# Performance work log

Hardware: AMD Instinct MI355X
Metric: run time of the kernel (lower is better)

The kernel has to match this reference:

```python
import jax, jax.numpy as jnp
import numpy as np

N_EMBD = 1024
N_HEAD = 16


def setup_inputs() -> dict:
    key = jax.random.key(0)
    ks = jax.random.split(key, 9)
    s = 1.0 / np.sqrt(N_EMBD)
    d = {
        "x": jax.random.normal(ks[0], (4, 2048, N_EMBD), dtype=jnp.float32),
        "Wq": jax.random.normal(ks[1], (N_EMBD, N_EMBD), dtype=jnp.float32) * s,
        "bq": jnp.zeros((N_EMBD,), dtype=jnp.float32),
        "Wk": jax.random.normal(ks[2], (N_EMBD, N_EMBD), dtype=jnp.float32) * s,
        "bk": jnp.zeros((N_EMBD,), dtype=jnp.float32),
        "Wv": jax.random.normal(ks[3], (N_EMBD, N_EMBD), dtype=jnp.float32) * s,
        "bv": jnp.zeros((N_EMBD,), dtype=jnp.float32),
        "Wp": jax.random.normal(ks[4], (N_EMBD, N_EMBD), dtype=jnp.float32) * s,
        "bp": jnp.zeros((N_EMBD,), dtype=jnp.float32),
    }
    return d


def reference(x, Wq, bq, Wk, bk, Wv, bv, Wp, bp):
    B, T, C = x.shape
    H = N_HEAD
    D = C // H  # head dim
    # QKV projections -> [B, H, T, D]
    def split_heads(y):
        return y.reshape(B, T, H, D).transpose(0, 2, 1, 3)
    q = split_heads(x @ Wq + bq)
    k = split_heads(x @ Wk + bk)
    v = split_heads(x @ Wv + bv)
    # full (non-causal) attention, scaled by 1/sqrt(D)
    att = jnp.einsum("bhtd,bhsd->bhts", q, k) * (1.0 / np.sqrt(D))
    att = jax.nn.softmax(att, axis=-1)  # dropout is identity (p=0 / eval)
    out = jnp.einsum("bhts,bhsd->bhtd", att, v)
    out = out.transpose(0, 2, 1, 3).reshape(B, T, C)
    return out @ Wp + bp
```

## Files before the change

### kernel.cpp

```cpp
#include <hip/hip_runtime.h>
#include <math.h>

#define B_ 4
#define T_ 2048
#define C_ 1024
#define H_ 16
#define D_ 64
#define M_ (B_ * T_)

#define QSCALE 0.18033688011112042f

using bf16x8 = __attribute__((ext_vector_type(8))) short;
using f32x4  = __attribute__((ext_vector_type(4))) float;

__device__ __forceinline__ unsigned short f2bf(float f) {
  unsigned u = __float_as_uint(f);
  unsigned r = u + 0x7FFFu + ((u >> 16) & 1u);
  return (unsigned short)(r >> 16);
}
__device__ __forceinline__ float bf2f(unsigned short h) {
  return __uint_as_float(((unsigned)h) << 16);
}

__global__ __launch_bounds__(256) void conv_x(const float* __restrict__ x,
                                              unsigned short* __restrict__ hi,
                                              unsigned short* __restrict__ lo) {
  const size_t i = ((size_t)blockIdx.x * 256 + threadIdx.x) * 4;
  const float4 v = *(const float4*)&x[i];
  ushort4 h, l;
  h.x = f2bf(v.x); l.x = f2bf(v.x - bf2f(h.x));
  h.y = f2bf(v.y); l.y = f2bf(v.y - bf2f(h.y));
  h.z = f2bf(v.z); l.z = f2bf(v.z - bf2f(h.z));
  h.w = f2bf(v.w); l.w = f2bf(v.w - bf2f(h.w));
  *(ushort4*)&hi[i] = h;
  *(ushort4*)&lo[i] = l;
}

__global__ __launch_bounds__(256) void conv_wT(const float* __restrict__ W,
                                               unsigned short* __restrict__ hi,
                                               unsigned short* __restrict__ lo,
                                               int n_off) {
  __shared__ float t[64][65];
  const int k0 = blockIdx.y * 64, n0 = blockIdx.x * 64;
  const int lr = threadIdx.x >> 4;
  const int lc4 = (threadIdx.x & 15) * 4;
#pragma unroll
  for (int i = 0; i < 4; ++i) {
    const int r = lr + 16 * i;
    const float4 v = *(const float4*)&W[(size_t)(k0 + r) * 1024 + n0 + lc4];
    t[r][lc4 + 0] = v.x; t[r][lc4 + 1] = v.y;
    t[r][lc4 + 2] = v.z; t[r][lc4 + 3] = v.w;
  }
  __syncthreads();
#pragma unroll
  for (int i = 0; i < 4; ++i) {
    const int nr = lr + 16 * i;
    ushort4 h, l;
    float a0 = t[lc4 + 0][nr], a1 = t[lc4 + 1][nr];
    float a2 = t[lc4 + 2][nr], a3 = t[lc4 + 3][nr];
    h.x = f2bf(a0); l.x = f2bf(a0 - bf2f(h.x));
    h.y = f2bf(a1); l.y = f2bf(a1 - bf2f(h.y));
    h.z = f2bf(a2); l.z = f2bf(a2 - bf2f(h.z));
    h.w = f2bf(a3); l.w = f2bf(a3 - bf2f(h.w));
    const size_t o = (size_t)(n_off + n0 + nr) * 1024 + k0 + lc4;
    *(ushort4*)&hi[o] = h;
    *(ushort4*)&lo[o] = l;
  }
}

template <int MODE>
__global__ __launch_bounds__(256) void gemm_mfma(
    const unsigned short* __restrict__ Ahi, const unsigned short* __restrict__ Alo,
    const unsigned short* __restrict__ Bhi, const unsigned short* __restrict__ Blo,
    const float* __restrict__ bias0, const float* __restrict__ bias1,
    const float* __restrict__ bias2,
    void* P0, void* P1, void* P2, void* P3, void* P4, void* P5) {
  __shared__ __align__(16) unsigned short Als[128 * 32];
  __shared__ __align__(16) unsigned short Bls[128 * 32];

  const int tid = threadIdx.x;
  const int lane = tid & 63;
  const int wid = tid >> 6;
  const int m0 = blockIdx.y * 128, n0 = blockIdx.x * 128;
  const int wm = (wid >> 1) * 64, wn = (wid & 1) * 64;

  f32x4 acc[4][4] = {};

  const int srow = lane >> 2;
  const int sc = lane & 3;

  for (int k0 = 0; k0 < 3 * 1024; k0 += 32) {
    const int seg = k0 >> 10;
    const int kk = k0 & 1023;
    const unsigned short* ga = (seg == 2) ? Alo : Ahi;
    const unsigned short* gb = (seg == 1) ? Blo : Bhi;

    __syncthreads();
#pragma unroll
    for (int c = 0; c < 2; ++c) {
      const int chunk = wid * 2 + c;
      const int row = chunk * 16 + srow;
      const int kch = sc ^ ((row >> 1) & 3);
      {
        const unsigned short* src = ga + (size_t)(m0 + row) * 1024 + kk + kch * 8;
        __builtin_amdgcn_global_load_lds(
            (const __attribute__((address_space(1))) void*)src,
            (__attribute__((address_space(3))) void*)(Als + chunk * 512), 16, 0, 0);
      }
      {
        const unsigned short* src = gb + (size_t)(n0 + row) * 1024 + kk + kch * 8;
        __builtin_amdgcn_global_load_lds(
            (const __attribute__((address_space(1))) void*)src,
            (__attribute__((address_space(3))) void*)(Bls + chunk * 512), 16, 0, 0);
      }
    }
    __syncthreads();

    const int fr = lane & 15;
    const int q = lane >> 4;
    bf16x8 af[4], bfr[4];
#pragma unroll
    for (int i = 0; i < 4; ++i) {
      const int arow = wm + i * 16 + fr;
      af[i] = *(const bf16x8*)(Als + arow * 32 + (q ^ ((arow >> 1) & 3)) * 8);
      const int brow = wn + i * 16 + fr;
      bfr[i] = *(const bf16x8*)(Bls + brow * 32 + (q ^ ((brow >> 1) & 3)) * 8);
    }
#pragma unroll
    for (int i = 0; i < 4; ++i)
#pragma unroll
      for (int j = 0; j < 4; ++j)
        acc[i][j] = __builtin_amdgcn_mfma_f32_16x16x32_bf16(af[i], bfr[j], acc[i][j], 0, 0, 0);
  }

  const int fr = lane & 15;
  const int q = lane >> 4;
  if (MODE == 0) {
    float* out = (float*)P0;
#pragma unroll
    for (int i = 0; i < 4; ++i)
#pragma unroll
      for (int j = 0; j < 4; ++j)
#pragma unroll
        for (int r = 0; r < 4; ++r) {
          const int m = m0 + wm + i * 16 + q * 4 + r;
          const int n = n0 + wn + j * 16 + fr;
          out[(size_t)m * 1024 + n] = acc[i][j][r] + bias0[n];
        }
  } else {
#pragma unroll
    for (int i = 0; i < 4; ++i) {
#pragma unroll
      for (int j = 0; j < 4; ++j) {
        const int n = n0 + wn + j * 16 + fr;
        const int seg = n >> 10, ww = n & 1023, h = ww >> 6, d = ww & 63;
        const float bv = ((seg == 0) ? bias0 : (seg == 1) ? bias1 : bias2)[ww];
        const int mb = m0 + wm + i * 16 + q * 4;
        const int b = mb >> 11, t0 = mb & 2047;
        unsigned short hv[4], lv[4];
#pragma unroll
        for (int r = 0; r < 4; ++r) {
          float v = acc[i][j][r] + bv;
          if (seg == 0) v *= QSCALE;
          hv[r] = f2bf(v);
          lv[r] = f2bf(v - bf2f(hv[r]));
        }
        if (seg == 2) {
          const size_t o = (((size_t)b * H_ + h) * D_ + d) * T_ + t0;
          ushort4 h4, l4;
          h4.x = hv[0]; h4.y = hv[1]; h4.z = hv[2]; h4.w = hv[3];
          l4.x = lv[0]; l4.y = lv[1]; l4.z = lv[2]; l4.w = lv[3];
          *(ushort4*)&((unsigned short*)P4)[o] = h4;
          *(ushort4*)&((unsigned short*)P5)[o] = l4;
        } else {
          unsigned short* Hq = (unsigned short*)((seg == 0) ? P0 : P2);
          unsigned short* Lq = (unsigned short*)((seg == 0) ? P1 : P3);
          const size_t ob = ((size_t)b * H_ + h) * T_;
#pragma unroll
          for (int r = 0; r < 4; ++r) {
            const size_t o = (ob + t0 + r) * D_ + d;
            Hq[o] = hv[r];
            Lq[o] = lv[r];
          }
        }
      }
    }
  }
}

__global__ __launch_bounds__(256) void flash_mfma(
    const unsigned short* __restrict__ Qhi, const unsigned short* __restrict__ Qlo,
    const unsigned short* __restrict__ Khi, const unsigned short* __restrict__ Klo,
    const unsigned short* __restrict__ Vthi, const unsigned short* __restrict__ Vtlo,
    unsigned short* __restrict__ chi, unsigned short* __restrict__ clo) {
  __shared__ __align__(16) unsigned short KhiS[64 * 64];
  __shared__ __align__(16) unsigned short KloS[64 * 64];
  __shared__ __align__(16) unsigned short VhiS[64 * 64];
  __shared__ __align__(16) unsigned short VloS[64 * 64];
  __shared__ __align__(16) unsigned short Ps[4][32][80];

  const int tid = threadIdx.x;
  const int lane = tid & 63;
  const int w = tid >> 6;
  const int bh = blockIdx.y;
  const int b = bh >> 4, h = bh & 15;
  const int q0 = blockIdx.x * 128;
  const int fr = lane & 15, q = lane >> 4;

  const size_t kbase = (size_t)bh * T_ * D_;
  const size_t vbase = (size_t)bh * D_ * T_;

  bf16x8 qhi[2][2], qlo[2][2];
#pragma unroll
  for (int g = 0; g < 2; ++g)
#pragma unroll
    for (int ks = 0; ks < 2; ++ks) {
      const size_t a = kbase + (size_t)(q0 + w * 32 + g * 16 + fr) * D_ + ks * 32 + q * 8;
      qhi[g][ks] = *(const bf16x8*)(Qhi + a);
      qlo[g][ks] = *(const bf16x8*)(Qlo + a);
    }

  f32x4 accO[2][4] = {};
  float lsum[2][4] = {};

  for (int s0 = 0; s0 < T_; s0 += 64) {
    __syncthreads();
#pragma unroll
    for (int c = 0; c < 2; ++c) {
      const int ci = w * 128 + c * 64 + lane;
      const int row = ci >> 3, slot = ci & 7;
      const int kch = slot ^ (row & 7);
      const int ldsb = (w * 128 + c * 64) * 8;
      const unsigned short* sk = Khi + kbase + (size_t)(s0 + row) * D_ + kch * 8;
      __builtin_amdgcn_global_load_lds(
          (const __attribute__((address_space(1))) void*)sk,
          (__attribute__((address_space(3))) void*)(KhiS + ldsb), 16, 0, 0);
      const unsigned short* sk2 = Klo + kbase + (size_t)(s0 + row) * D_ + kch * 8;
      __builtin_amdgcn_global_load_lds(
          (const __attribute__((address_space(1))) void*)sk2,
          (__attribute__((address_space(3))) void*)(KloS + ldsb), 16, 0, 0);
      const unsigned short* sv = Vthi + vbase + (size_t)row * T_ + s0 + kch * 8;
      __builtin_amdgcn_global_load_lds(
          (const __attribute__((address_space(1))) void*)sv,
          (__attribute__((address_space(3))) void*)(VhiS + ldsb), 16, 0, 0);
      const unsigned short* sv2 = Vtlo + vbase + (size_t)row * T_ + s0 + kch * 8;
      __builtin_amdgcn_global_load_lds(
          (const __attribute__((address_space(1))) void*)sv2,
          (__attribute__((address_space(3))) void*)(VloS + ldsb), 16, 0, 0);
    }
    __syncthreads();

    f32x4 accS[2][4] = {};
#pragma unroll
    for (int j = 0; j < 4; ++j) {
      bf16x8 khf[2], klf[2];
#pragma unroll
      for (int ks = 0; ks < 2; ++ks) {
        const int rs = j * 16 + fr;
        const int off = rs * 64 + ((ks * 4 + q) ^ (rs & 7)) * 8;
        khf[ks] = *(const bf16x8*)(KhiS + off);
        klf[ks] = *(const bf16x8*)(KloS + off);
      }
#pragma unroll
      for (int g = 0; g < 2; ++g)
#pragma unroll
        for (int ks = 0; ks < 2; ++ks) {
          accS[g][j] = __builtin_amdgcn_mfma_f32_16x16x32_bf16(qhi[g][ks], khf[ks], accS[g][j], 0, 0, 0);
          accS[g][j] = __builtin_amdgcn_mfma_f32_16x16x32_bf16(qhi[g][ks], klf[ks], accS[g][j], 0, 0, 0);
          accS[g][j] = __builtin_amdgcn_mfma_f32_16x16x32_bf16(qlo[g][ks], khf[ks], accS[g][j], 0, 0, 0);
        }
    }

#pragma unroll
    for (int g = 0; g < 2; ++g)
#pragma unroll
      for (int j = 0; j < 4; ++j)
#pragma unroll
        for (int r = 0; r < 4; ++r) {
          const float p = __builtin_amdgcn_exp2f(accS[g][j][r]);
          lsum[g][r] += p;
          Ps[w][g * 16 + q * 4 + r][j * 16 + fr] = f2bf(p);
        }

    asm volatile("s_waitcnt lgkmcnt(0)" ::: "memory");
    __builtin_amdgcn_sched_barrier(0);

    bf16x8 pa[2][2];
#pragma unroll
    for (int g = 0; g < 2; ++g)
#pragma unroll
      for (int ks = 0; ks < 2; ++ks)
        pa[g][ks] = *(const bf16x8*)&Ps[w][g * 16 + fr][ks * 32 + q * 8];
#pragma unroll
    for (int j = 0; j < 4; ++j) {
      bf16x8 vh[2], vl[2];
#pragma unroll
      for (int ks = 0; ks < 2; ++ks) {
        const int rd = j * 16 + fr;
        const int off = rd * 64 + ((ks * 4 + q) ^ (rd & 7)) * 8;
        vh[ks] = *(const bf16x8*)(VhiS + off);
        vl[ks] = *(const bf16x8*)(VloS + off);
      }
#pragma unroll
      for (int g = 0; g < 2; ++g)
#pragma unroll
        for (int ks = 0; ks < 2; ++ks) {
          accO[g][j] = __builtin_amdgcn_mfma_f32_16x16x32_bf16(pa[g][ks], vh[ks], accO[g][j], 0, 0, 0);
          accO[g][j] = __builtin_amdgcn_mfma_f32_16x16x32_bf16(pa[g][ks], vl[ks], accO[g][j], 0, 0, 0);
        }
    }
  }

#pragma unroll
  for (int g = 0; g < 2; ++g) {
#pragma unroll
    for (int r = 0; r < 4; ++r) {
      float rs = lsum[g][r];
#pragma unroll
      for (int off = 1; off < 16; off <<= 1) rs += __shfl_xor(rs, off);
      const float inv = 1.0f / rs;
      const int t = q0 + w * 32 + g * 16 + q * 4 + r;
#pragma unroll
      for (int j = 0; j < 4; ++j) {
        const float v = accO[g][j][r] * inv;
        const unsigned short hv = f2bf(v);
        const unsigned short lv = f2bf(v - bf2f(hv));
        const size_t idx = ((size_t)b * T_ + t) * C_ + h * D_ + j * 16 + fr;
        chi[idx] = hv;
        clo[idx] = lv;
      }
    }
  }
}

extern "C" void kernel_launch(void* const* d_in, const int* in_sizes, int n_in,
                              void* d_out, int out_size, void* d_ws,
                              size_t ws_size, hipStream_t stream) {
  const float* x = (const float*)d_in[0];
  const float* Wq = (const float*)d_in[1];
  const float* bq = (const float*)d_in[2];
  const float* Wk = (const float*)d_in[3];
  const float* bk = (const float*)d_in[4];
  const float* Wv = (const float*)d_in[5];
  const float* bv = (const float*)d_in[6];
  const float* Wp = (const float*)d_in[7];
  const float* bp = (const float*)d_in[8];
  float* out = (float*)d_out;

  char* w = (char*)d_ws;
  unsigned short* xhi = (unsigned short*)w;     w += (size_t)M_ * C_ * 2;
  unsigned short* xlo = (unsigned short*)w;     w += (size_t)M_ * C_ * 2;
  unsigned short* Wqkv_hi = (unsigned short*)w; w += (size_t)3 * C_ * C_ * 2;
  unsigned short* Wqkv_lo = (unsigned short*)w; w += (size_t)3 * C_ * C_ * 2;
  unsigned short* Wp_hi = (unsigned short*)w;   w += (size_t)C_ * C_ * 2;
  unsigned short* Wp_lo = (unsigned short*)w;   w += (size_t)C_ * C_ * 2;
  unsigned short* Qhi = (unsigned short*)w;     w += (size_t)M_ * C_ * 2;
  unsigned short* Qlo = (unsigned short*)w;     w += (size_t)M_ * C_ * 2;
  unsigned short* Khi = (unsigned short*)w;     w += (size_t)M_ * C_ * 2;
  unsigned short* Klo = (unsigned short*)w;     w += (size_t)M_ * C_ * 2;
  unsigned short* Vthi = (unsigned short*)w;    w += (size_t)M_ * C_ * 2;
  unsigned short* Vtlo = (unsigned short*)w;    w += (size_t)M_ * C_ * 2;
  unsigned short* chi = (unsigned short*)w;     w += (size_t)M_ * C_ * 2;
  unsigned short* clo = (unsigned short*)w;     w += (size_t)M_ * C_ * 2;

  const dim3 blk(256);

  conv_x<<<dim3((M_ * C_) / (4 * 256)), blk, 0, stream>>>(x, xhi, xlo);
  conv_wT<<<dim3(16, 16), blk, 0, stream>>>(Wq, Wqkv_hi, Wqkv_lo, 0);
  conv_wT<<<dim3(16, 16), blk, 0, stream>>>(Wk, Wqkv_hi, Wqkv_lo, 1024);
  conv_wT<<<dim3(16, 16), blk, 0, stream>>>(Wv, Wqkv_hi, Wqkv_lo, 2048);
  conv_wT<<<dim3(16, 16), blk, 0, stream>>>(Wp, Wp_hi, Wp_lo, 0);

  gemm_mfma<1><<<dim3(3072 / 128, M_ / 128), blk, 0, stream>>>(
      xhi, xlo, Wqkv_hi, Wqkv_lo, bq, bk, bv,
      Qhi, Qlo, Khi, Klo, Vthi, Vtlo);

  flash_mfma<<<dim3(T_ / 128, B_ * H_), blk, 0, stream>>>(
      Qhi, Qlo, Khi, Klo, Vthi, Vtlo, chi, clo);

  gemm_mfma<0><<<dim3(1024 / 128, M_ / 128), blk, 0, stream>>>(
      chi, clo, Wp_hi, Wp_lo, bp, bp, bp,
      out, nullptr, nullptr, nullptr, nullptr, nullptr);

  (void)in_sizes; (void)n_in; (void)out_size; (void)ws_size;
}
```

Before: 552.9 us.

## Merge split-bf16 GEMM passes, swizzle block order, transpose attention MFMA operands

The GEMM now loads hi and lo tiles of A and B together and runs all three bf16 products in one K loop. A and B tiles are staged once instead of three times, at the cost of doubling LDS use and raising register pressure. Both the GEMM and the flash kernel remap block indices so neighbouring workgroups share data in cache. The flash kernel swaps MFMA operands to compute transposed S and O tiles, which allows packed bf16 conversion of P, swizzled P stores to LDS, a cheaper row-sum reduction and vectorised output stores.

```diff
diff --git a/kernel.cpp b/kernel.cpp
--- a/kernel.cpp
+++ b/kernel.cpp
@@ -20,6 +20,11 @@
 }
 __device__ __forceinline__ float bf2f(unsigned short h) {
   return __uint_as_float(((unsigned)h) << 16);
+}
+__device__ __forceinline__ unsigned cvtpk_bf16(float lo, float hi) {
+  unsigned r;
+  asm volatile("v_cvt_pk_bf16_f32 %0, %1, %2" : "=v"(r) : "v"(lo), "v"(hi));
+  return r;
 }
 
 __global__ __launch_bounds__(256) void conv_x(const float* __restrict__ x,
@@ -75,66 +80,91 @@
     const float* __restrict__ bias0, const float* __restrict__ bias1,
     const float* __restrict__ bias2,
     void* P0, void* P1, void* P2, void* P3, void* P4, void* P5) {
-  __shared__ __align__(16) unsigned short Als[128 * 32];
-  __shared__ __align__(16) unsigned short Bls[128 * 32];
+  __shared__ __align__(16) unsigned short AhS[128 * 32];
+  __shared__ __align__(16) unsigned short AlS[128 * 32];
+  __shared__ __align__(16) unsigned short BhS[128 * 32];
+  __shared__ __align__(16) unsigned short BlS[128 * 32];
 
   const int tid = threadIdx.x;
   const int lane = tid & 63;
   const int wid = tid >> 6;
-  const int m0 = blockIdx.y * 128, n0 = blockIdx.x * 128;
+
+  const int GX = (MODE == 1) ? 24 : 8;
+  const int nwg = GX * 64;
+  int lin = blockIdx.x + blockIdx.y * GX;
+  lin = (lin & 7) * (nwg >> 3) + (lin >> 3);
+  const int m0 = (lin / GX) * 128, n0 = (lin % GX) * 128;
+
   const int wm = (wid >> 1) * 64, wn = (wid & 1) * 64;
 
   f32x4 acc[4][4] = {};
 
   const int srow = lane >> 2;
   const int sc = lane & 3;
-
-  for (int k0 = 0; k0 < 3 * 1024; k0 += 32) {
-    const int seg = k0 >> 10;
-    const int kk = k0 & 1023;
-    const unsigned short* ga = (seg == 2) ? Alo : Ahi;
-    const unsigned short* gb = (seg == 1) ? Blo : Bhi;
-
+  const int fr = lane & 15;
+  const int q = lane >> 4;
+
+  for (int k0 = 0; k0 < 1024; k0 += 32) {
     __syncthreads();
 #pragma unroll
     for (int c = 0; c < 2; ++c) {
       const int chunk = wid * 2 + c;
       const int row = chunk * 16 + srow;
       const int kch = sc ^ ((row >> 1) & 3);
-      {
-        const unsigned short* src = ga + (size_t)(m0 + row) * 1024 + kk + kch * 8;
-        __builtin_amdgcn_global_load_lds(
-            (const __attribute__((address_space(1))) void*)src,
-            (__attribute__((address_space(3))) void*)(Als + chunk * 512), 16, 0, 0);
-      }
-      {
-        const unsigned short* src = gb + (size_t)(n0 + row) * 1024 + kk + kch * 8;
-        __builtin_amdgcn_global_load_lds(
-            (const __attribute__((address_space(1))) void*)src,
-            (__attribute__((address_space(3))) void*)(Bls + chunk * 512), 16, 0, 0);
-      }
+      const size_t ao = (size_t)(m0 + row) * 1024 + k0 + kch * 8;
+      const size_t bo = (size_t)(n0 + row) * 1024 + k0 + kch * 8;
+      __builtin_amdgcn_global_load_lds(
+          (const __attribute__((address_space(1))) void*)(Ahi + ao),
+          (__attribute__((address_space(3))) void*)(AhS + chunk * 512), 16, 0, 0);
+      __builtin_amdgcn_global_load_lds(
+          (const __attribute__((address_space(1))) void*)(Alo + ao),
+          (__attribute__((address_space(3))) void*)(AlS + chunk * 512), 16, 0, 0);
+      __builtin_amdgcn_global_load_lds(
+          (const __attribute__((address_space(1))) void*)(Bhi + bo),
+          (__attribute__((address_space(3))) void*)(BhS + chunk * 512), 16, 0, 0);
+      __builtin_amdgcn_global_load_lds(
+          (const __attribute__((address_space(1))) void*)(Blo + bo),
+          (__attribute__((address_space(3))) void*)(BlS + chunk * 512), 16, 0, 0);
     }
     __syncthreads();
 
-    const int fr = lane & 15;
-    const int q = lane >> 4;
-    bf16x8 af[4], bfr[4];
+    bf16x8 afh[4], bfh[4], afl[4], bfl[4];
 #pragma unroll
     for (int i = 0; i < 4; ++i) {
       const int arow = wm + i * 16 + fr;
-      af[i] = *(const bf16x8*)(Als + arow * 32 + (q ^ ((arow >> 1) & 3)) * 8);
+      const int aoff = arow * 32 + (q ^ ((arow >> 1) & 3)) * 8;
+      afh[i] = *(const bf16x8*)(AhS + aoff);
       const int brow = wn + i * 16 + fr;
-      bfr[i] = *(const bf16x8*)(Bls + brow * 32 + (q ^ ((brow >> 1) & 3)) * 8);
+      const int boff = brow * 32 + (q ^ ((brow >> 1) & 3)) * 8;
+      bfh[i] = *(const bf16x8*)(BhS + boff);
     }
 #pragma unroll
     for (int i = 0; i < 4; ++i)
 #pragma unroll
       for (int j = 0; j < 4; ++j)
-        acc[i][j] = __builtin_amdgcn_mfma_f32_16x16x32_bf16(af[i], bfr[j], acc[i][j], 0, 0, 0);
-  }
-
-  const int fr = lane & 15;
-  const int q = lane >> 4;
+        acc[i][j] = __builtin_amdgcn_mfma_f32_16x16x32_bf16(afh[i], bfh[j], acc[i][j], 0, 0, 0);
+#pragma unroll
+    for (int i = 0; i < 4; ++i) {
+      const int brow = wn + i * 16 + fr;
+      bfl[i] = *(const bf16x8*)(BlS + brow * 32 + (q ^ ((brow >> 1) & 3)) * 8);
+    }
+#pragma unroll
+    for (int i = 0; i < 4; ++i)
+#pragma unroll
+      for (int j = 0; j < 4; ++j)
+        acc[i][j] = __builtin_amdgcn_mfma_f32_16x16x32_bf16(afh[i], bfl[j], acc[i][j], 0, 0, 0);
+#pragma unroll
+    for (int i = 0; i < 4; ++i) {
+      const int arow = wm + i * 16 + fr;
+      afl[i] = *(const bf16x8*)(AlS + arow * 32 + (q ^ ((arow >> 1) & 3)) * 8);
+    }
+#pragma unroll
+    for (int i = 0; i < 4; ++i)
+#pragma unroll
+      for (int j = 0; j < 4; ++j)
+        acc[i][j] = __builtin_amdgcn_mfma_f32_16x16x32_bf16(afl[i], bfh[j], acc[i][j], 0, 0, 0);
+  }
+
   if (MODE == 0) {
     float* out = (float*)P0;
 #pragma unroll
@@ -197,14 +227,18 @@
   __shared__ __align__(16) unsigned short KloS[64 * 64];
   __shared__ __align__(16) unsigned short VhiS[64 * 64];
   __shared__ __align__(16) unsigned short VloS[64 * 64];
-  __shared__ __align__(16) unsigned short Ps[4][32][80];
+  __shared__ __align__(16) unsigned short PsT[4][32 * 64];
 
   const int tid = threadIdx.x;
   const int lane = tid & 63;
   const int w = tid >> 6;
-  const int bh = blockIdx.y;
+
+  int lin = blockIdx.x + blockIdx.y * 16;
+  lin = (lin & 7) * 128 + (lin >> 3);
+  const int bh = lin >> 4;
+  const int q0 = (lin & 15) * 128;
+
   const int b = bh >> 4, h = bh & 15;
-  const int q0 = blockIdx.x * 128;
   const int fr = lane & 15, q = lane >> 4;
 
   const size_t kbase = (size_t)bh * T_ * D_;
@@ -220,8 +254,10 @@
       qlo[g][ks] = *(const bf16x8*)(Qlo + a);
     }
 
-  f32x4 accO[2][4] = {};
-  float lsum[2][4] = {};
+  unsigned short* psw = &PsT[w][0];
+
+  f32x4 accO[4][2] = {};
+  float lsum[2] = {};
 
   for (int s0 = 0; s0 < T_; s0 += 64) {
     __syncthreads();
@@ -250,13 +286,13 @@
     }
     __syncthreads();
 
-    f32x4 accS[2][4] = {};
-#pragma unroll
-    for (int j = 0; j < 4; ++j) {
+    f32x4 accS[4][2] = {};
+#pragma unroll
+    for (int sj = 0; sj < 4; ++sj) {
       bf16x8 khf[2], klf[2];
 #pragma unroll
       for (int ks = 0; ks < 2; ++ks) {
-        const int rs = j * 16 + fr;
+        const int rs = sj * 16 + fr;
         const int off = rs * 64 + ((ks * 4 + q) ^ (rs & 7)) * 8;
         khf[ks] = *(const bf16x8*)(KhiS + off);
         klf[ks] = *(const bf16x8*)(KloS + off);
@@ -265,32 +301,41 @@
       for (int g = 0; g < 2; ++g)
 #pragma unroll
         for (int ks = 0; ks < 2; ++ks) {
-          accS[g][j] = __builtin_amdgcn_mfma_f32_16x16x32_bf16(qhi[g][ks], khf[ks], accS[g][j], 0, 0, 0);
-          accS[g][j] = __builtin_amdgcn_mfma_f32_16x16x32_bf16(qhi[g][ks], klf[ks], accS[g][j], 0, 0, 0);
-          accS[g][j] = __builtin_amdgcn_mfma_f32_16x16x32_bf16(qlo[g][ks], khf[ks], accS[g][j], 0, 0, 0);
+          accS[sj][g] = __builtin_amdgcn_mfma_f32_16x16x32_bf16(khf[ks], qhi[g][ks], accS[sj][g], 0, 0, 0);
+          accS[sj][g] = __builtin_amdgcn_mfma_f32_16x16x32_bf16(khf[ks], qlo[g][ks], accS[sj][g], 0, 0, 0);
+          accS[sj][g] = __builtin_amdgcn_mfma_f32_16x16x32_bf16(klf[ks], qhi[g][ks], accS[sj][g], 0, 0, 0);
         }
     }
 
 #pragma unroll
-    for (int g = 0; g < 2; ++g)
-#pragma unroll
-      for (int j = 0; j < 4; ++j)
-#pragma unroll
-        for (int r = 0; r < 4; ++r) {
-          const float p = __builtin_amdgcn_exp2f(accS[g][j][r]);
-          lsum[g][r] += p;
-          Ps[w][g * 16 + q * 4 + r][j * 16 + fr] = f2bf(p);
-        }
+    for (int g = 0; g < 2; ++g) {
+      const int qc = g * 16 + fr;
+#pragma unroll
+      for (int sj = 0; sj < 4; ++sj) {
+        const float p0 = __builtin_amdgcn_exp2f(accS[sj][g][0]);
+        const float p1 = __builtin_amdgcn_exp2f(accS[sj][g][1]);
+        const float p2 = __builtin_amdgcn_exp2f(accS[sj][g][2]);
+        const float p3 = __builtin_amdgcn_exp2f(accS[sj][g][3]);
+        lsum[g] += (p0 + p1) + (p2 + p3);
+        uint2 pk;
+        pk.x = cvtpk_bf16(p0, p1);
+        pk.y = cvtpk_bf16(p2, p3);
+        const int off = (qc * 128 + sj * 32 + q * 8) ^ ((fr & 7) << 4);
+        *(uint2*)((char*)psw + off) = pk;
+      }
+    }
 
     asm volatile("s_waitcnt lgkmcnt(0)" ::: "memory");
     __builtin_amdgcn_sched_barrier(0);
 
-    bf16x8 pa[2][2];
+    bf16x8 pb[2][2];
 #pragma unroll
     for (int g = 0; g < 2; ++g)
 #pragma unroll
-      for (int ks = 0; ks < 2; ++ks)
-        pa[g][ks] = *(const bf16x8*)&Ps[w][g * 16 + fr][ks * 32 + q * 8];
+      for (int ks = 0; ks < 2; ++ks) {
+        const int off = ((g * 16 + fr) * 128 + ks * 64 + q * 16) ^ ((fr & 7) << 4);
+        pb[g][ks] = *(const bf16x8*)((char*)psw + off);
+      }
 #pragma unroll
     for (int j = 0; j < 4; ++j) {
       bf16x8 vh[2], vl[2];
@@ -305,30 +350,32 @@
       for (int g = 0; g < 2; ++g)
 #pragma unroll
         for (int ks = 0; ks < 2; ++ks) {
-          accO[g][j] = __builtin_amdgcn_mfma_f32_16x16x32_bf16(pa[g][ks], vh[ks], accO[g][j], 0, 0, 0);
-          accO[g][j] = __builtin_amdgcn_mfma_f32_16x16x32_bf16(pa[g][ks], vl[ks], accO[g][j], 0, 0, 0);
+          accO[j][g] = __builtin_amdgcn_mfma_f32_16x16x32_bf16(vh[ks], pb[g][ks], accO[j][g], 0, 0, 0);
+          accO[j][g] = __builtin_amdgcn_mfma_f32_16x16x32_bf16(vl[ks], pb[g][ks], accO[j][g], 0, 0, 0);
         }
     }
   }
 
 #pragma unroll
   for (int g = 0; g < 2; ++g) {
-#pragma unroll
-    for (int r = 0; r < 4; ++r) {
-      float rs = lsum[g][r];
-#pragma unroll
-      for (int off = 1; off < 16; off <<= 1) rs += __shfl_xor(rs, off);
-      const float inv = 1.0f / rs;
-      const int t = q0 + w * 32 + g * 16 + q * 4 + r;
-#pragma unroll
-      for (int j = 0; j < 4; ++j) {
-        const float v = accO[g][j][r] * inv;
-        const unsigned short hv = f2bf(v);
-        const unsigned short lv = f2bf(v - bf2f(hv));
-        const size_t idx = ((size_t)b * T_ + t) * C_ + h * D_ + j * 16 + fr;
-        chi[idx] = hv;
-        clo[idx] = lv;
-      }
+    float rs = lsum[g];
+    rs += __shfl_xor(rs, 16);
+    rs += __shfl_xor(rs, 32);
+    const float inv = 1.0f / rs;
+    const int t = q0 + w * 32 + g * 16 + fr;
+    const size_t rowb = ((size_t)b * T_ + t) * C_ + h * D_;
+#pragma unroll
+    for (int j = 0; j < 4; ++j) {
+      ushort4 h4, l4;
+      float v0 = accO[j][g][0] * inv, v1 = accO[j][g][1] * inv;
+      float v2 = accO[j][g][2] * inv, v3 = accO[j][g][3] * inv;
+      h4.x = f2bf(v0); l4.x = f2bf(v0 - bf2f(h4.x));
+      h4.y = f2bf(v1); l4.y = f2bf(v1 - bf2f(h4.y));
+      h4.z = f2bf(v2); l4.z = f2bf(v2 - bf2f(h4.z));
+      h4.w = f2bf(v3); l4.w = f2bf(v3 - bf2f(h4.w));
+      const size_t idx = rowb + j * 16 + q * 4;
+      *(ushort4*)&chi[idx] = h4;
+      *(ushort4*)&clo[idx] = l4;
     }
   }
 }
```

Result: faster. 522.3 us (-5.5%).
